# Kernel tuning notes

Hardware: AMD Instinct MI355X
Metric: run time of the kernel (lower is better)

Reference implementation:

```python
import jax, jax.numpy as jnp
import numpy as np

N_NODES = 100000
N_EDGES = 250000
N_GRAPHS = 512
VOCAB = 1000
EMBED = 256
HIDDEN = 512
OUT = 128
EPS = 1e-5


def setup_inputs() -> dict:
    key = jax.random.key(0)
    ks = jax.random.split(key, 16)
    s = 0.02
    return {
        "x": jax.random.randint(ks[0], (N_NODES, 1), 0, VOCAB),
        "edge_index": jax.random.randint(ks[1], (2, N_EDGES), 0, N_NODES),
        "batch": jnp.sort(jax.random.randint(ks[2], (N_NODES,), 0, N_GRAPHS)),
        "emb": jax.random.normal(ks[3], (VOCAB, EMBED), jnp.float32) * s,
        "W1": jax.random.normal(ks[4], (EMBED, HIDDEN), jnp.float32) * s,
        "b1": jnp.zeros((HIDDEN,), jnp.float32),
        "g1": jnp.ones((HIDDEN,), jnp.float32),
        "be1": jnp.zeros((HIDDEN,), jnp.float32),
        "W2": jax.random.normal(ks[5], (HIDDEN, HIDDEN), jnp.float32) * s,
        "b2": jnp.zeros((HIDDEN,), jnp.float32),
        "g2": jnp.ones((HIDDEN,), jnp.float32),
        "be2": jnp.zeros((HIDDEN,), jnp.float32),
        "Wl1": jax.random.normal(ks[6], (HIDDEN, HIDDEN // 2), jnp.float32) * s,
        "bl1": jnp.zeros((HIDDEN // 2,), jnp.float32),
        "Wl2": jax.random.normal(ks[7], (HIDDEN // 2, OUT), jnp.float32) * s,
        "bl2": jnp.zeros((OUT,), jnp.float32),
    }


def _mpnn(h, edge_index, W, b):
    # sum-aggregate messages x_j from source to target, plus self-loop, then linear
    src, dst = edge_index[0], edge_index[1]
    agg = jax.ops.segment_sum(h[src], dst, num_segments=h.shape[0]) + h
    return agg @ W + b


def _bn(h, g, be):
    # BatchNorm1d, training-mode batch statistics (biased variance)
    mu = jnp.mean(h, axis=0)
    var = jnp.mean(jnp.square(h - mu), axis=0)
    return (h - mu) * jax.lax.rsqrt(var + EPS) * g + be


def reference(x, edge_index, batch, emb, W1, b1, g1, be1, W2, b2, g2, be2, Wl1, bl1, Wl2, bl2):
    h = emb[x[:, 0]]                                   # [N, EMBED]
    h = jax.nn.relu(_bn(_mpnn(h, edge_index, W1, b1), g1, be1))
    h = jax.nn.relu(_bn(_mpnn(h, edge_index, W2, b2), g2, be2))
    # global mean pool per graph
    sums = jax.ops.segment_sum(h, batch, num_segments=N_GRAPHS)
    cnts = jax.ops.segment_sum(jnp.ones((h.shape[0],), h.dtype), batch, num_segments=N_GRAPHS)
    pooled = sums / jnp.maximum(cnts, 1.0)[:, None]    # [G, HIDDEN]
    z = jax.nn.relu(pooled @ Wl1 + bl1)                # dropout is identity in eval
    return z @ Wl2 + bl2                               # [G, OUT]
```

## Files before the change

kernel.cpp:

```cpp
#include <hip/hip_runtime.h>
#include <cstdint>
#include <cstddef>

#define N_NODES 100000
#define N_EDGES 250000
#define N_GRAPHS 512
#define MTILES 782
#define MPAD (MTILES * 128)
#define SB 256
#define NBLK ((N_NODES + SB - 1) / SB)
#define GEMM_BLOCKS 3136

using f32x4  = __attribute__((ext_vector_type(4))) float;
using bf16x8 = __attribute__((ext_vector_type(8))) short;

struct alignas(8) U16x4 { unsigned short x, y, z, w; };

__device__ __forceinline__ unsigned short f32_to_bf16(float f) {
    union { float f; uint32_t u; } v; v.f = f;
    uint32_t r = v.u + 0x7FFF + ((v.u >> 16) & 1);
    return (unsigned short)(r >> 16);
}
__device__ __forceinline__ float bf_lo(uint32_t u) {
    union { uint32_t u; float f; } v; v.u = u << 16; return v.f;
}
__device__ __forceinline__ float bf_hi(uint32_t u) {
    union { uint32_t u; float f; } v; v.u = u & 0xFFFF0000u; return v.f;
}

__device__ __forceinline__ void async_cp16(const void* g, void* l) {
    __builtin_amdgcn_global_load_lds(
        (const __attribute__((address_space(1))) void*)g,
        (__attribute__((address_space(3))) void*)l, 16, 0, 0);
}

__global__ void k_zero_int(int* __restrict__ p, int n) {
    int i = blockIdx.x * 256 + threadIdx.x;
    if (i < n) p[i] = 0;
}
__global__ void k_zero_f(float* __restrict__ p, int n) {
    int i = blockIdx.x * 256 + threadIdx.x;
    if (i < n) p[i] = 0.f;
}

__global__ void k_hist(const int* __restrict__ ei, int* __restrict__ counts) {
    int e = blockIdx.x * 256 + threadIdx.x;
    if (e < N_EDGES) atomicAdd(&counts[ei[N_EDGES + e]], 1);
}

__global__ __launch_bounds__(SB) void k_blocksum(const int* __restrict__ counts,
                                                 int* __restrict__ bsum) {
    __shared__ int red[4];
    int i = blockIdx.x * SB + threadIdx.x;
    int v = (i < N_NODES) ? counts[i] : 0;
#pragma unroll
    for (int off = 1; off < 64; off <<= 1) v += __shfl_xor(v, off);
    int wave = threadIdx.x >> 6, lane = threadIdx.x & 63;
    if (lane == 0) red[wave] = v;
    __syncthreads();
    if (threadIdx.x == 0) bsum[blockIdx.x] = red[0] + red[1] + red[2] + red[3];
}

__global__ __launch_bounds__(512) void k_scan_bsum(const int* __restrict__ bsum,
                                                   int* __restrict__ bpre) {
    __shared__ int s[512];
    int t = threadIdx.x;
    int orig = (t < NBLK) ? bsum[t] : 0;
    s[t] = orig;
    __syncthreads();
    for (int off = 1; off < 512; off <<= 1) {
        int v = (t >= off) ? s[t - off] : 0;
        __syncthreads();
        s[t] += v;
        __syncthreads();
    }
    if (t < NBLK) bpre[t] = s[t] - orig;
}

__global__ __launch_bounds__(SB) void k_scan_final(const int* __restrict__ counts,
                                                   const int* __restrict__ bpre,
                                                   int* __restrict__ rowptr,
                                                   int* __restrict__ cursor) {
    __shared__ int s[SB];
    int t = threadIdx.x;
    int i = blockIdx.x * SB + t;
    int c = (i < N_NODES) ? counts[i] : 0;
    s[t] = c;
    __syncthreads();
    for (int off = 1; off < SB; off <<= 1) {
        int v = (t >= off) ? s[t - off] : 0;
        __syncthreads();
        s[t] += v;
        __syncthreads();
    }
    int pre = bpre[blockIdx.x] + s[t] - c;
    if (i < N_NODES) { rowptr[i] = pre; cursor[i] = pre; }
    if (i == 0) rowptr[N_NODES] = N_EDGES;
}

__global__ void k_fill(const int* __restrict__ ei, int* __restrict__ cursor,
                       int* __restrict__ srcs) {
    int e = blockIdx.x * 256 + threadIdx.x;
    if (e < N_EDGES) {
        int dst = ei[N_EDGES + e];
        int p = atomicAdd(&cursor[dst], 1);
        srcs[p] = ei[e];
    }
}

__global__ __launch_bounds__(256) void k_gather1(
    const int* __restrict__ x, const float* __restrict__ emb,
    const int* __restrict__ rowptr, const int* __restrict__ srcs,
    unsigned short* __restrict__ agg1b) {
    int wave = threadIdx.x >> 6, lane = threadIdx.x & 63;
    int node = blockIdx.x * 4 + wave;
    if (node >= N_NODES) return;
    int row = x[node];
    float4 acc = ((const float4*)emb)[(size_t)row * 64 + lane];
    int j0 = rowptr[node], j1 = rowptr[node + 1];
    for (int j = j0; j < j1; ++j) {
        int s = srcs[j];
        int r = x[s];
        float4 v = ((const float4*)emb)[(size_t)r * 64 + lane];
        acc.x += v.x; acc.y += v.y; acc.z += v.z; acc.w += v.w;
    }
    U16x4 o{ f32_to_bf16(acc.x), f32_to_bf16(acc.y), f32_to_bf16(acc.z), f32_to_bf16(acc.w) };
    ((U16x4*)agg1b)[(size_t)node * 64 + lane] = o;
}

#define SLAB_LD 136
template <int K>
__global__ __launch_bounds__(256) void k_gemm_bias_stats(
    const unsigned short* __restrict__ A, const unsigned short* __restrict__ Bt,
    const float* __restrict__ bias, unsigned short* __restrict__ Cb,
    float* __restrict__ colsum, float* __restrict__ colsq, int M) {
    __shared__ __align__(16) unsigned short sh[16384];
    unsigned short* lA = sh;
    unsigned short* lB = sh + 8192;
    const int tid  = threadIdx.x;
    const int wave = tid >> 6, lane = tid & 63;
    const int b = blockIdx.x;
    const int m0 = ((b >> 5) * 8 + (b & 7)) * 128;
    const int n0 = ((b & 31) >> 3) * 128;
    if (m0 >= M) return;
    const int wr = (wave >> 1) * 64;
    const int wc = (wave & 1) * 64;
    const int quad = lane >> 4, m16 = lane & 15;

    f32x4 acc[4][4] = {};

    for (int k0 = 0; k0 < K; k0 += 64) {
        __syncthreads();
#pragma unroll
        for (int t = 0; t < 4; ++t) {
            int seg = (wave * 4 + t) * 64 + lane;
            int row = seg >> 3, csl = seg & 7;
            int cs  = csl ^ (row & 7);
            const unsigned short* gA = A + (size_t)(m0 + row) * K + (k0 + cs * 8);
            async_cp16(gA, &lA[seg * 8]);
            const unsigned short* gB = Bt + (size_t)(n0 + row) * K + (k0 + cs * 8);
            async_cp16(gB, &lB[seg * 8]);
        }
        __syncthreads();

#pragma unroll
        for (int h = 0; h < 2; ++h) {
            bf16x8 af[4], bfr[4];
#pragma unroll
            for (int rb = 0; rb < 4; ++rb) {
                int r = wr + rb * 16 + m16;
                int g = (h * 4 + quad) ^ (r & 7);
                af[rb] = *(const bf16x8*)&lA[r * 64 + g * 8];
            }
#pragma unroll
            for (int cb = 0; cb < 4; ++cb) {
                int r = wc + cb * 16 + m16;
                int g = (h * 4 + quad) ^ (r & 7);
                bfr[cb] = *(const bf16x8*)&lB[r * 64 + g * 8];
            }
#pragma unroll
            for (int rb = 0; rb < 4; ++rb)
#pragma unroll
                for (int cb = 0; cb < 4; ++cb)
                    acc[rb][cb] = __builtin_amdgcn_mfma_f32_16x16x32_bf16(
                        af[rb], bfr[cb], acc[rb][cb], 0, 0, 0);
        }
    }

    float bvs[4];
#pragma unroll
    for (int cb = 0; cb < 4; ++cb) {
        int col = n0 + wc + cb * 16 + m16;
        float bv = bias[col];
        bvs[cb] = bv;
        float s = 0.f, s2 = 0.f;
#pragma unroll
        for (int rb = 0; rb < 4; ++rb) {
#pragma unroll
            for (int i = 0; i < 4; ++i) {
                int row = m0 + wr + rb * 16 + quad * 4 + i;
                if (row < M) {
                    float v = acc[rb][cb][i] + bv;
                    s += v; s2 += v * v;
                }
            }
        }
        s  += __shfl_xor(s, 16);   s  += __shfl_xor(s, 32);
        s2 += __shfl_xor(s2, 16);  s2 += __shfl_xor(s2, 32);
        if (quad == 0) {
            atomicAdd(&colsum[col], s);
            atomicAdd(&colsq[col], s2);
        }
    }

#pragma unroll
    for (int rb = 0; rb < 4; ++rb) {
        __syncthreads();
#pragma unroll
        for (int cb = 0; cb < 4; ++cb) {
            int scol = wc + cb * 16 + m16;
#pragma unroll
            for (int i = 0; i < 4; ++i) {
                int sr = (wave >> 1) * 16 + quad * 4 + i;
                sh[sr * SLAB_LD + scol] = f32_to_bf16(acc[rb][cb][i] + bvs[cb]);
            }
        }
        __syncthreads();
#pragma unroll
        for (int s = 0; s < 2; ++s) {
            int u = tid + s * 256;
            int sr = u >> 4, c8 = u & 15;
            int gr = m0 + (sr >> 4) * 64 + rb * 16 + (sr & 15);
            uint4 v = *(const uint4*)&sh[sr * SLAB_LD + c8 * 8];
            *(uint4*)&Cb[(size_t)gr * 512 + n0 + c8 * 8] = v;
        }
    }
}

__global__ void k_cvt_wt(const float* __restrict__ W, unsigned short* __restrict__ Wt,
                         int K, int N) {
    int i = blockIdx.x * 256 + threadIdx.x;
    if (i < K * N) {
        int k = i / N, n = i - k * N;
        Wt[(size_t)n * K + k] = f32_to_bf16(W[i]);
    }
}

__global__ void k_bn_coeffs(const float* __restrict__ colsum, const float* __restrict__ colsq,
                            const float* __restrict__ g, const float* __restrict__ be,
                            float* __restrict__ a, float* __restrict__ c) {
    int f = blockIdx.x * 256 + threadIdx.x;
    if (f >= 512) return;
    float mu  = colsum[f] * (1.f / N_NODES);
    float var = colsq[f] * (1.f / N_NODES) - mu * mu;
    float ai  = g[f] * rsqrtf(var + 1e-5f);
    a[f] = ai;
    c[f] = be[f] - mu * ai;
}

__global__ __launch_bounds__(256) void k_gather2(
    const unsigned short* __restrict__ pre1b, const int* __restrict__ rowptr,
    const int* __restrict__ srcs, const float* __restrict__ a1,
    const float* __restrict__ c1, unsigned short* __restrict__ agg2b) {
    int wave = threadIdx.x >> 6, lane = threadIdx.x & 63;
    int node = blockIdx.x * 4 + wave;
    if (node >= N_NODES) return;
    float4 aa0 = ((const float4*)a1)[lane * 2], aa1 = ((const float4*)a1)[lane * 2 + 1];
    float4 cc0 = ((const float4*)c1)[lane * 2], cc1 = ((const float4*)c1)[lane * 2 + 1];
    float acc[8] = {};
    int j0 = rowptr[node], j1 = rowptr[node + 1];
    for (int j = j0 - 1; j < j1; ++j) {
        int s = (j < j0) ? node : srcs[j];
        uint4 raw = ((const uint4*)(pre1b + (size_t)s * 512))[lane];
        acc[0] += fmaxf(fmaf(aa0.x, bf_lo(raw.x), cc0.x), 0.f);
        acc[1] += fmaxf(fmaf(aa0.y, bf_hi(raw.x), cc0.y), 0.f);
        acc[2] += fmaxf(fmaf(aa0.z, bf_lo(raw.y), cc0.z), 0.f);
        acc[3] += fmaxf(fmaf(aa0.w, bf_hi(raw.y), cc0.w), 0.f);
        acc[4] += fmaxf(fmaf(aa1.x, bf_lo(raw.z), cc1.x), 0.f);
        acc[5] += fmaxf(fmaf(aa1.y, bf_hi(raw.z), cc1.y), 0.f);
        acc[6] += fmaxf(fmaf(aa1.z, bf_lo(raw.w), cc1.z), 0.f);
        acc[7] += fmaxf(fmaf(aa1.w, bf_hi(raw.w), cc1.w), 0.f);
    }
    U16x4 o0{ f32_to_bf16(acc[0]), f32_to_bf16(acc[1]), f32_to_bf16(acc[2]), f32_to_bf16(acc[3]) };
    U16x4 o1{ f32_to_bf16(acc[4]), f32_to_bf16(acc[5]), f32_to_bf16(acc[6]), f32_to_bf16(acc[7]) };
    ((U16x4*)agg2b)[(size_t)node * 128 + lane * 2]     = o0;
    ((U16x4*)agg2b)[(size_t)node * 128 + lane * 2 + 1] = o1;
}

__global__ void k_seg_starts(const int* __restrict__ batch, int* __restrict__ starts) {
    int i = blockIdx.x * 256 + threadIdx.x;
    if (i >= N_NODES) return;
    int b = batch[i];
    if (i == 0) {
        for (int g = 0; g <= b; ++g) starts[g] = 0;
    } else {
        int p = batch[i - 1];
        for (int g = p + 1; g <= b; ++g) starts[g] = i;
    }
    if (i == N_NODES - 1) {
        for (int g = b + 1; g <= N_GRAPHS; ++g) starts[g] = N_NODES;
    }
}

__global__ __launch_bounds__(256) void k_pool(const unsigned short* __restrict__ pre2b,
                                              const int* __restrict__ starts,
                                              const float* __restrict__ a2,
                                              const float* __restrict__ c2,
                                              float* __restrict__ pooled) {
    __shared__ float red[3 * 512];
    int g = blockIdx.x;
    int wave = threadIdx.x >> 6, lane = threadIdx.x & 63;
    int s = starts[g], e = starts[g + 1];
    float4 aa0 = ((const float4*)a2)[lane * 2], aa1 = ((const float4*)a2)[lane * 2 + 1];
    float4 cc0 = ((const float4*)c2)[lane * 2], cc1 = ((const float4*)c2)[lane * 2 + 1];
    float acc[8] = {};
    for (int n = s + wave; n < e; n += 4) {
        uint4 raw = ((const uint4*)(pre2b + (size_t)n * 512))[lane];
        acc[0] += fmaxf(fmaf(aa0.x, bf_lo(raw.x), cc0.x), 0.f);
        acc[1] += fmaxf(fmaf(aa0.y, bf_hi(raw.x), cc0.y), 0.f);
        acc[2] += fmaxf(fmaf(aa0.z, bf_lo(raw.y), cc0.z), 0.f);
        acc[3] += fmaxf(fmaf(aa0.w, bf_hi(raw.y), cc0.w), 0.f);
        acc[4] += fmaxf(fmaf(aa1.x, bf_lo(raw.z), cc1.x), 0.f);
        acc[5] += fmaxf(fmaf(aa1.y, bf_hi(raw.z), cc1.y), 0.f);
        acc[6] += fmaxf(fmaf(aa1.z, bf_lo(raw.w), cc1.z), 0.f);
        acc[7] += fmaxf(fmaf(aa1.w, bf_hi(raw.w), cc1.w), 0.f);
    }
    if (wave != 0) {
#pragma unroll
        for (int j = 0; j < 8; ++j) red[(wave - 1) * 512 + lane * 8 + j] = acc[j];
    }
    __syncthreads();
    if (wave == 0) {
#pragma unroll
        for (int j = 0; j < 8; ++j)
            acc[j] += red[lane * 8 + j] + red[512 + lane * 8 + j] + red[1024 + lane * 8 + j];
        float inv = 1.f / fmaxf((float)(e - s), 1.f);
#pragma unroll
        for (int j = 0; j < 8; ++j) pooled[(size_t)g * 512 + lane * 8 + j] = acc[j] * inv;
    }
}

__global__ __launch_bounds__(256) void k_mlp1(const float* __restrict__ pooled,
                                              const float* __restrict__ Wl1,
                                              const float* __restrict__ bl1,
                                              float* __restrict__ z) {
    __shared__ float sp[512];
    int i = blockIdx.x, j = threadIdx.x;
    sp[j]       = pooled[(size_t)i * 512 + j];
    sp[j + 256] = pooled[(size_t)i * 512 + 256 + j];
    __syncthreads();
    float acc = bl1[j];
#pragma unroll 4
    for (int k = 0; k < 512; ++k) acc = fmaf(sp[k], Wl1[(size_t)k * 256 + j], acc);
    z[(size_t)i * 256 + j] = fmaxf(acc, 0.f);
}

__global__ __launch_bounds__(128) void k_mlp2(const float* __restrict__ z,
                                              const float* __restrict__ Wl2,
                                              const float* __restrict__ bl2,
                                              float* __restrict__ out) {
    __shared__ float sz[256];
    int i = blockIdx.x, j = threadIdx.x;
    sz[j]       = z[(size_t)i * 256 + j];
    sz[j + 128] = z[(size_t)i * 256 + 128 + j];
    __syncthreads();
    float acc = bl2[j];
#pragma unroll 4
    for (int k = 0; k < 256; ++k) acc = fmaf(sz[k], Wl2[(size_t)k * 128 + j], acc);
    out[(size_t)i * 128 + j] = acc;
}

extern "C" void kernel_launch(void* const* d_in, const int* in_sizes, int n_in,
                              void* d_out, int out_size, void* d_ws, size_t ws_size,
                              hipStream_t stream) {
    const int*   x    = (const int*)d_in[0];
    const int*   ei   = (const int*)d_in[1];
    const int*   batch= (const int*)d_in[2];
    const float* emb  = (const float*)d_in[3];
    const float* W1   = (const float*)d_in[4];
    const float* b1   = (const float*)d_in[5];
    const float* g1   = (const float*)d_in[6];
    const float* be1  = (const float*)d_in[7];
    const float* W2   = (const float*)d_in[8];
    const float* b2   = (const float*)d_in[9];
    const float* g2   = (const float*)d_in[10];
    const float* be2  = (const float*)d_in[11];
    const float* Wl1  = (const float*)d_in[12];
    const float* bl1  = (const float*)d_in[13];
    const float* Wl2  = (const float*)d_in[14];
    const float* bl2  = (const float*)d_in[15];
    float* out = (float*)d_out;

    char* ws = (char*)d_ws;
    size_t o = 0;
    auto alloc = [&](size_t bytes) { char* p = ws + o; o += (bytes + 255) & ~(size_t)255; return p; };

    unsigned short* W1tb = (unsigned short*)alloc((size_t)512 * 256 * 2);
    unsigned short* W2tb = (unsigned short*)alloc((size_t)512 * 512 * 2);
    float* sums   = (float*)alloc(4 * 512 * 4);
    float* colsum1 = sums, *colsq1 = sums + 512, *colsum2 = sums + 1024, *colsq2 = sums + 1536;
    float* coeffs = (float*)alloc(4 * 512 * 4);
    float* a1 = coeffs, *c1 = coeffs + 512, *a2 = coeffs + 1024, *c2 = coeffs + 1536;
    int*   starts = (int*)alloc((N_GRAPHS + 1) * 4);
    float* pooled = (float*)alloc((size_t)N_GRAPHS * 512 * 4);
    float* zbuf   = (float*)alloc((size_t)N_GRAPHS * 256 * 4);
    int*   counts = (int*)alloc((size_t)N_NODES * 4);
    int*   rowptr = (int*)alloc((size_t)(N_NODES + 1) * 4);
    int*   cursor = (int*)alloc((size_t)N_NODES * 4);
    int*   srcs   = (int*)alloc((size_t)N_EDGES * 4);
    int*   bsum   = (int*)alloc((size_t)NBLK * 4);
    int*   bpre   = (int*)alloc((size_t)NBLK * 4);

    char* slotA = alloc((size_t)MPAD * 512 * 2);
    unsigned short* agg1b = (unsigned short*)slotA;
    unsigned short* agg2b = (unsigned short*)slotA;
    char* slotB = alloc((size_t)MPAD * 512 * 2);
    unsigned short* pre1b = (unsigned short*)slotB;
    unsigned short* pre2b = (unsigned short*)slotB;
    (void)ws_size; (void)in_sizes; (void)n_in; (void)out_size;

    k_zero_int<<<(N_NODES + 255) / 256, 256, 0, stream>>>(counts, N_NODES);
    k_zero_f<<<8, 256, 0, stream>>>(sums, 2048);
    k_hist<<<(N_EDGES + 255) / 256, 256, 0, stream>>>(ei, counts);
    k_blocksum<<<NBLK, SB, 0, stream>>>(counts, bsum);
    k_scan_bsum<<<1, 512, 0, stream>>>(bsum, bpre);
    k_scan_final<<<NBLK, SB, 0, stream>>>(counts, bpre, rowptr, cursor);
    k_fill<<<(N_EDGES + 255) / 256, 256, 0, stream>>>(ei, cursor, srcs);

    k_cvt_wt<<<(256 * 512 + 255) / 256, 256, 0, stream>>>(W1, W1tb, 256, 512);
    k_cvt_wt<<<(512 * 512 + 255) / 256, 256, 0, stream>>>(W2, W2tb, 512, 512);

    k_gather1<<<(N_NODES + 3) / 4, 256, 0, stream>>>(x, emb, rowptr, srcs, agg1b);
    k_gemm_bias_stats<256><<<GEMM_BLOCKS, 256, 0, stream>>>(
        agg1b, W1tb, b1, pre1b, colsum1, colsq1, N_NODES);
    k_bn_coeffs<<<2, 256, 0, stream>>>(colsum1, colsq1, g1, be1, a1, c1);

    k_gather2<<<(N_NODES + 3) / 4, 256, 0, stream>>>(pre1b, rowptr, srcs, a1, c1, agg2b);
    k_gemm_bias_stats<512><<<GEMM_BLOCKS, 256, 0, stream>>>(
        agg2b, W2tb, b2, pre2b, colsum2, colsq2, N_NODES);
    k_bn_coeffs<<<2, 256, 0, stream>>>(colsum2, colsq2, g2, be2, a2, c2);

    k_seg_starts<<<(N_NODES + 255) / 256, 256, 0, stream>>>(batch, starts);
    k_pool<<<N_GRAPHS, 256, 0, stream>>>(pre2b, starts, a2, c2, pooled);
    k_mlp1<<<N_GRAPHS, 256, 0, stream>>>(pooled, Wl1, bl1, zbuf);
    k_mlp2<<<N_GRAPHS, 128, 0, stream>>>(zbuf, Wl2, bl2, out);
}
```

Measured before the change: 477.1 us.

## Precompute embedding-times-W1 table and gather projected rows for layer one

Because layer one is linear over embedding rows, the change multiplies the 1000-row embedding table by W1 once (a small GEMM padded to 1024 rows), then gathers and sums projected 512-wide rows per node, adding bias and accumulating BN statistics in a fused gather kernel. This removes the 100k-row layer-one GEMM and the intermediate agg1 buffer write and read. In exchange each gathered row is 512 bf16 values instead of 256 fp32 values, and rounding happens before the sum rather than after, which slightly changes numerics. Column statistics are reduced across waves in shared memory before the atomics.

New measurement: 597.0 us. 1.25x slower.

```diff
diff --git a/kernel.cpp b/kernel.cpp
--- a/kernel.cpp
+++ b/kernel.cpp
@@ -10,6 +10,7 @@
 #define SB 256
 #define NBLK ((N_NODES + SB - 1) / SB)
 #define GEMM_BLOCKS 3136
+#define NPB 128
 
 using f32x4  = __attribute__((ext_vector_type(4))) float;
 using bf16x8 = __attribute__((ext_vector_type(8))) short;
@@ -108,28 +109,8 @@
     }
 }
 
-__global__ __launch_bounds__(256) void k_gather1(
-    const int* __restrict__ x, const float* __restrict__ emb,
-    const int* __restrict__ rowptr, const int* __restrict__ srcs,
-    unsigned short* __restrict__ agg1b) {
-    int wave = threadIdx.x >> 6, lane = threadIdx.x & 63;
-    int node = blockIdx.x * 4 + wave;
-    if (node >= N_NODES) return;
-    int row = x[node];
-    float4 acc = ((const float4*)emb)[(size_t)row * 64 + lane];
-    int j0 = rowptr[node], j1 = rowptr[node + 1];
-    for (int j = j0; j < j1; ++j) {
-        int s = srcs[j];
-        int r = x[s];
-        float4 v = ((const float4*)emb)[(size_t)r * 64 + lane];
-        acc.x += v.x; acc.y += v.y; acc.z += v.z; acc.w += v.w;
-    }
-    U16x4 o{ f32_to_bf16(acc.x), f32_to_bf16(acc.y), f32_to_bf16(acc.z), f32_to_bf16(acc.w) };
-    ((U16x4*)agg1b)[(size_t)node * 64 + lane] = o;
-}
-
 #define SLAB_LD 136
-template <int K>
+template <int K, bool STATS>
 __global__ __launch_bounds__(256) void k_gemm_bias_stats(
     const unsigned short* __restrict__ A, const unsigned short* __restrict__ Bt,
     const float* __restrict__ bias, unsigned short* __restrict__ Cb,
@@ -191,25 +172,27 @@
 #pragma unroll
     for (int cb = 0; cb < 4; ++cb) {
         int col = n0 + wc + cb * 16 + m16;
-        float bv = bias[col];
+        float bv = STATS ? bias[col] : 0.f;
         bvs[cb] = bv;
-        float s = 0.f, s2 = 0.f;
-#pragma unroll
-        for (int rb = 0; rb < 4; ++rb) {
-#pragma unroll
-            for (int i = 0; i < 4; ++i) {
-                int row = m0 + wr + rb * 16 + quad * 4 + i;
-                if (row < M) {
-                    float v = acc[rb][cb][i] + bv;
-                    s += v; s2 += v * v;
+        if constexpr (STATS) {
+            float s = 0.f, s2 = 0.f;
+#pragma unroll
+            for (int rb = 0; rb < 4; ++rb) {
+#pragma unroll
+                for (int i = 0; i < 4; ++i) {
+                    int row = m0 + wr + rb * 16 + quad * 4 + i;
+                    if (row < M) {
+                        float v = acc[rb][cb][i] + bv;
+                        s += v; s2 += v * v;
+                    }
                 }
             }
-        }
-        s  += __shfl_xor(s, 16);   s  += __shfl_xor(s, 32);
-        s2 += __shfl_xor(s2, 16);  s2 += __shfl_xor(s2, 32);
-        if (quad == 0) {
-            atomicAdd(&colsum[col], s);
-            atomicAdd(&colsq[col], s2);
+            s  += __shfl_xor(s, 16);   s  += __shfl_xor(s, 32);
+            s2 += __shfl_xor(s2, 16);  s2 += __shfl_xor(s2, 32);
+            if (quad == 0) {
+                atomicAdd(&colsum[col], s);
+                atomicAdd(&colsq[col], s2);
+            }
         }
     }
 
@@ -244,6 +227,11 @@
         int k = i / N, n = i - k * N;
         Wt[(size_t)n * K + k] = f32_to_bf16(W[i]);
     }
+}
+
+__global__ void k_cvt_emb(const float* __restrict__ e, unsigned short* __restrict__ o) {
+    int i = blockIdx.x * 256 + threadIdx.x;
+    if (i < 1000 * 256) o[i] = f32_to_bf16(e[i]);
 }
 
 __global__ void k_bn_coeffs(const float* __restrict__ colsum, const float* __restrict__ colsq,
@@ -256,6 +244,57 @@
     float ai  = g[f] * rsqrtf(var + 1e-5f);
     a[f] = ai;
     c[f] = be[f] - mu * ai;
+}
+
+__global__ __launch_bounds__(256) void k_gather_pre1(
+    const unsigned short* __restrict__ embW, const int* __restrict__ x,
+    const int* __restrict__ rowptr, const int* __restrict__ srcs,
+    const float* __restrict__ b1, unsigned short* __restrict__ pre1b,
+    float* __restrict__ colsum, float* __restrict__ colsq) {
+    __shared__ float red[2][3][512];
+    int wave = threadIdx.x >> 6, lane = threadIdx.x & 63;
+    float4 bl = ((const float4*)b1)[lane * 2], bh = ((const float4*)b1)[lane * 2 + 1];
+    float ssum[8] = {}, ssq[8] = {};
+    int base = blockIdx.x * NPB + wave * (NPB / 4);
+    for (int t = 0; t < NPB / 4; ++t) {
+        int node = base + t;
+        if (node >= N_NODES) break;
+        float acc[8] = { bl.x, bl.y, bl.z, bl.w, bh.x, bh.y, bh.z, bh.w };
+        int j0 = rowptr[node], j1 = rowptr[node + 1];
+        for (int j = j0 - 1; j < j1; ++j) {
+            int s = (j < j0) ? node : srcs[j];
+            int r = x[s];
+            uint4 raw = ((const uint4*)(embW + (size_t)r * 512))[lane];
+            acc[0] += bf_lo(raw.x); acc[1] += bf_hi(raw.x);
+            acc[2] += bf_lo(raw.y); acc[3] += bf_hi(raw.y);
+            acc[4] += bf_lo(raw.z); acc[5] += bf_hi(raw.z);
+            acc[6] += bf_lo(raw.w); acc[7] += bf_hi(raw.w);
+        }
+        U16x4 o0{ f32_to_bf16(acc[0]), f32_to_bf16(acc[1]), f32_to_bf16(acc[2]), f32_to_bf16(acc[3]) };
+        U16x4 o1{ f32_to_bf16(acc[4]), f32_to_bf16(acc[5]), f32_to_bf16(acc[6]), f32_to_bf16(acc[7]) };
+        ((U16x4*)pre1b)[(size_t)node * 128 + lane * 2]     = o0;
+        ((U16x4*)pre1b)[(size_t)node * 128 + lane * 2 + 1] = o1;
+#pragma unroll
+        for (int j2 = 0; j2 < 8; ++j2) { ssum[j2] += acc[j2]; ssq[j2] += acc[j2] * acc[j2]; }
+    }
+    if (wave != 0) {
+#pragma unroll
+        for (int j2 = 0; j2 < 8; ++j2) {
+            red[0][wave - 1][lane * 8 + j2] = ssum[j2];
+            red[1][wave - 1][lane * 8 + j2] = ssq[j2];
+        }
+    }
+    __syncthreads();
+    if (wave == 0) {
+#pragma unroll
+        for (int j2 = 0; j2 < 8; ++j2) {
+            int col = lane * 8 + j2;
+            float s  = ssum[j2] + red[0][0][col] + red[0][1][col] + red[0][2][col];
+            float s2 = ssq[j2]  + red[1][0][col] + red[1][1][col] + red[1][2][col];
+            atomicAdd(&colsum[col], s);
+            atomicAdd(&colsq[col], s2);
+        }
+    }
 }
 
 __global__ __launch_bounds__(256) void k_gather2(
@@ -397,6 +436,8 @@
 
     unsigned short* W1tb = (unsigned short*)alloc((size_t)512 * 256 * 2);
     unsigned short* W2tb = (unsigned short*)alloc((size_t)512 * 512 * 2);
+    unsigned short* embB = (unsigned short*)alloc((size_t)1024 * 256 * 2);
+    unsigned short* embW = (unsigned short*)alloc((size_t)1024 * 512 * 2);
     float* sums   = (float*)alloc(4 * 512 * 4);
     float* colsum1 = sums, *colsq1 = sums + 512, *colsum2 = sums + 1024, *colsq2 = sums + 1536;
     float* coeffs = (float*)alloc(4 * 512 * 4);
@@ -411,9 +452,7 @@
     int*   bsum   = (int*)alloc((size_t)NBLK * 4);
     int*   bpre   = (int*)alloc((size_t)NBLK * 4);
 
-    char* slotA = alloc((size_t)MPAD * 512 * 2);
-    unsigned short* agg1b = (unsigned short*)slotA;
-    unsigned short* agg2b = (unsigned short*)slotA;
+    unsigned short* agg2b = (unsigned short*)alloc((size_t)MPAD * 512 * 2);
     char* slotB = alloc((size_t)MPAD * 512 * 2);
     unsigned short* pre1b = (unsigned short*)slotB;
     unsigned short* pre2b = (unsigned short*)slotB;
@@ -429,14 +468,16 @@
 
     k_cvt_wt<<<(256 * 512 + 255) / 256, 256, 0, stream>>>(W1, W1tb, 256, 512);
     k_cvt_wt<<<(512 * 512 + 255) / 256, 256, 0, stream>>>(W2, W2tb, 512, 512);
-
-    k_gather1<<<(N_NODES + 3) / 4, 256, 0, stream>>>(x, emb, rowptr, srcs, agg1b);
-    k_gemm_bias_stats<256><<<GEMM_BLOCKS, 256, 0, stream>>>(
-        agg1b, W1tb, b1, pre1b, colsum1, colsq1, N_NODES);
+    k_cvt_emb<<<1000, 256, 0, stream>>>(emb, embB);
+    k_gemm_bias_stats<256, false><<<32, 256, 0, stream>>>(
+        embB, W1tb, nullptr, embW, nullptr, nullptr, 1024);
+
+    k_gather_pre1<<<(N_NODES + NPB - 1) / NPB, 256, 0, stream>>>(
+        embW, x, rowptr, srcs, b1, pre1b, colsum1, colsq1);
     k_bn_coeffs<<<2, 256, 0, stream>>>(colsum1, colsq1, g1, be1, a1, c1);
 
     k_gather2<<<(N_NODES + 3) / 4, 256, 0, stream>>>(pre1b, rowptr, srcs, a1, c1, agg2b);
-    k_gemm_bias_stats<512><<<GEMM_BLOCKS, 256, 0, stream>>>(
+    k_gemm_bias_stats<512, true><<<GEMM_BLOCKS, 256, 0, stream>>>(
         agg2b, W2tb, b2, pre2b, colsum2, colsq2, N_NODES);
     k_bn_coeffs<<<2, 256, 0, stream>>>(colsum2, colsq2, g2, be2, a2, c2);
 
```
